# Performance work log

Hardware: AMD Instinct MI355X
Metric: run time of the kernel (lower is better)

## Reference

```python
import jax, jax.numpy as jnp
import numpy as np

N = 100000
DEG = 16            # edges per source node (1 self-loop + 15 random)
E = N * DEG
IN_F = 128
OUT_F = 64
ALPHA = 0.2         # leaky relu negative slope


def _build_edges(key):
    # edges sorted by src (as adj.nonzero() would be), every node has >=1 out-edge
    src = jnp.repeat(jnp.arange(N, dtype=jnp.int32), DEG)
    dst = jax.random.randint(key, (E,), 0, N, dtype=jnp.int32)
    # force a self-loop as the first edge of every block
    self_pos = jnp.arange(E, dtype=jnp.int32) % DEG == 0
    dst = jnp.where(self_pos, src, dst)
    return jnp.stack([src, dst])  # [2, E]


def setup_inputs() -> dict:
    key = jax.random.key(0)
    k1, k2, k3, k4, k5, k6 = jax.random.split(key, 6)
    return {
        "input": jax.random.normal(k1, (N, IN_F), dtype=jnp.float32),
        "edge": _build_edges(k2),
        "W_high": jax.random.normal(k3, (IN_F, OUT_F), dtype=jnp.float32) * 0.1,
        "W_low": jax.random.normal(k4, (IN_F, OUT_F), dtype=jnp.float32) * 0.1,
        "a_high": jax.random.normal(k5, (1, 2 * OUT_F), dtype=jnp.float32) * 0.1,
        "a_low": jax.random.normal(k6, (1, 2 * OUT_F), dtype=jnp.float32) * 0.1,
    }


def _relu6(x):
    return jnp.clip(x, 0.0, 6.0)


def reference(input, edge, W_high, W_low, a_high, a_low):
    n = input.shape[0]
    src, dst = edge[0], edge[1]

    h_high = input @ W_high          # [N, F]
    h_low = input @ W_low            # [N, F]

    # a.mm(cat(h[src], h[dst]).T) == (h @ a_src)[src] + (h @ a_dst)[dst]
    f = W_high.shape[1]
    s_high = (h_high @ a_high[0, :f])[src] + (h_high @ a_high[0, f:])[dst]  # [E]
    s_low = (h_low @ a_low[0, :f])[src] + (h_low @ a_low[0, f:])[dst]

    edge_e_high = jnp.exp(-jax.nn.leaky_relu(s_high, ALPHA))  # [E], > 0
    edge_e_low = jnp.exp(-jax.nn.leaky_relu(s_low, ALPHA))

    seg = lambda v: jax.ops.segment_sum(v, src, num_segments=n, indices_are_sorted=True)

    # rowsum uses RAW exp values (before relu6/dropout), matching the source
    e_high_rowsum = seg(edge_e_high)[:, None]  # [N, 1]
    e_low_rowsum = seg(edge_e_low)[:, None]

    # relu6 clamp (dropout p=0 -> identity, eval mode)
    eh = _relu6(edge_e_high)
    el = _relu6(edge_e_low)

    # m @ (h[src] +/- h[dst]) == segment_sum over src of per-edge features
    h_agg_high = seg(h_high[src] + h_high[dst])   # [N, F]
    h_agg_low = seg(h_low[src] - h_low[dst])      # [N, F]

    # spmm: out[i] = sum_{(i,j)} e_ij * h_agg[j]
    h_prime_high = seg(eh[:, None] * h_agg_high[dst]) / e_high_rowsum
    h_prime_low = seg(el[:, None] * h_agg_low[dst]) / e_low_rowsum

    h_prime = 0.5 * (h_prime_high + h_prime_low)
    return _relu6(h_prime)  # concat=True
```

## Files before the change

kernel.cpp:

```cpp
#include <hip/hip_runtime.h>

#define N_NODES 100000
#define DEG 16
#define IN_F 128
#define OUT_F 64
#define E_EDGES (N_NODES * DEG)

typedef __bf16 bf16x8 __attribute__((ext_vector_type(8)));
typedef unsigned short u16x8 __attribute__((ext_vector_type(8)));
typedef float f32x4 __attribute__((ext_vector_type(4)));

union BF8 { u16x8 u; bf16x8 b; };

__device__ inline float bf2f(unsigned short u) {
    union { unsigned int i; float f; } v; v.i = ((unsigned int)u) << 16; return v.f;
}
__device__ inline unsigned short f2bf(float f) {
    union { float f; unsigned int i; } v; v.f = f;
    unsigned int r = (v.i + 0x7FFFu + ((v.i >> 16) & 1u)) >> 16;
    return (unsigned short)r;
}

__global__ __launch_bounds__(256) void k_gemm(
    const float* __restrict__ in, const float* __restrict__ Wh,
    const float* __restrict__ Wl, unsigned short* __restrict__ h_high,
    unsigned short* __restrict__ h_low)
{
    __shared__ unsigned short ldsW[2][64][136];
    for (int idx = threadIdx.x; idx < IN_F * OUT_F; idx += 256) {
        int k = idx >> 6, n = idx & 63;
        ldsW[0][n][k] = f2bf(Wh[idx]);
        ldsW[1][n][k] = f2bf(Wl[idx]);
    }
    __syncthreads();

    int wave = blockIdx.x * 4 + (threadIdx.x >> 6);
    int lane = threadIdx.x & 63;
    int row0 = wave * 16;
    if (row0 >= N_NODES) return;

    int quad = lane >> 4;
    int mrow = row0 + (lane & 15);
    int lrow = mrow < N_NODES ? mrow : (N_NODES - 1);

    bf16x8 afrag[4];
    const float* inrow = in + (size_t)lrow * IN_F + quad * 8;
    #pragma unroll
    for (int kb = 0; kb < 4; kb++) {
        f32x4 v0 = *(const f32x4*)(inrow + kb * 32);
        f32x4 v1 = *(const f32x4*)(inrow + kb * 32 + 4);
        bf16x8 a;
        #pragma unroll
        for (int j = 0; j < 4; j++) { a[j] = (__bf16)v0[j]; a[4 + j] = (__bf16)v1[j]; }
        afrag[kb] = a;
    }

    f32x4 acc[2][4];
    #pragma unroll
    for (int m = 0; m < 2; m++)
        #pragma unroll
        for (int ct = 0; ct < 4; ct++) acc[m][ct] = (f32x4){0, 0, 0, 0};

    #pragma unroll
    for (int kb = 0; kb < 4; kb++) {
        #pragma unroll
        for (int ct = 0; ct < 4; ct++) {
            int n = ct * 16 + (lane & 15);
            BF8 bh, bl;
            bh.u = *(const u16x8*)&ldsW[0][n][kb * 32 + quad * 8];
            bl.u = *(const u16x8*)&ldsW[1][n][kb * 32 + quad * 8];
            acc[0][ct] = __builtin_amdgcn_mfma_f32_16x16x32_bf16(afrag[kb], bh.b, acc[0][ct], 0, 0, 0);
            acc[1][ct] = __builtin_amdgcn_mfma_f32_16x16x32_bf16(afrag[kb], bl.b, acc[1][ct], 0, 0, 0);
        }
    }

    #pragma unroll
    for (int r = 0; r < 4; r++) {
        int row = row0 + quad * 4 + r;
        if (row >= N_NODES) continue;
        size_t base = (size_t)row * OUT_F + (lane & 15);
        #pragma unroll
        for (int ct = 0; ct < 4; ct++) {
            h_high[base + ct * 16] = f2bf(acc[0][ct][r]);
            h_low [base + ct * 16] = f2bf(acc[1][ct][r]);
        }
    }
}

__global__ __launch_bounds__(256) void k_agg(
    const unsigned short* __restrict__ h_high, const unsigned short* __restrict__ h_low,
    const int* __restrict__ dst, const float* __restrict__ ah, const float* __restrict__ al,
    unsigned short* __restrict__ hagg_h, unsigned short* __restrict__ hagg_l,
    f32x4* __restrict__ s)
{
    int node = blockIdx.x * 4 + (threadIdx.x >> 6);
    if (node >= N_NODES) return;
    int lane = threadIdx.x & 63;

    int jl = dst[node * DEG + (lane & 15)];
    float hh = bf2f(h_high[(size_t)node * 64 + lane]);
    float hl = bf2f(h_low [(size_t)node * 64 + lane]);

    float sh = 16.0f * hh;
    float sl = 16.0f * hl;
    #pragma unroll
    for (int e = 0; e < DEG; e++) {
        int j = __shfl(jl, e);
        sh += bf2f(h_high[(size_t)j * 64 + lane]);
        sl -= bf2f(h_low [(size_t)j * 64 + lane]);
    }
    hagg_h[(size_t)node * 64 + lane] = f2bf(sh);
    hagg_l[(size_t)node * 64 + lane] = f2bf(sl);

    float ph = hh * ah[lane];
    float qh = hh * ah[64 + lane];
    float pl = hl * al[lane];
    float ql = hl * al[64 + lane];
    #pragma unroll
    for (int o = 32; o > 0; o >>= 1) {
        ph += __shfl_xor(ph, o);
        qh += __shfl_xor(qh, o);
        pl += __shfl_xor(pl, o);
        ql += __shfl_xor(ql, o);
    }
    if (lane == 0) s[node] = (f32x4){ph, qh, pl, ql};
}

__global__ __launch_bounds__(256) void k_out(
    const unsigned short* __restrict__ hagg_h, const unsigned short* __restrict__ hagg_l,
    const int* __restrict__ dst, const f32x4* __restrict__ s,
    float* __restrict__ out)
{
    int node = blockIdx.x * 4 + (threadIdx.x >> 6);
    if (node >= N_NODES) return;
    int lane = threadIdx.x & 63;

    int jl = dst[node * DEG + (lane & 15)];
    f32x4 si = s[node];
    float acc_h = 0.0f, acc_l = 0.0f, rs_h = 0.0f, rs_l = 0.0f;
    #pragma unroll
    for (int e = 0; e < DEG; e++) {
        int j = __shfl(jl, e);
        f32x4 sj = s[j];
        float xh = si.x + sj.y;
        float xl = si.z + sj.w;
        float lh = xh > 0.0f ? xh : 0.2f * xh;
        float ll = xl > 0.0f ? xl : 0.2f * xl;
        float wh = __expf(-lh);
        float wl = __expf(-ll);
        rs_h += wh;
        rs_l += wl;
        float eh = fminf(wh, 6.0f);
        float el = fminf(wl, 6.0f);
        acc_h += eh * bf2f(hagg_h[(size_t)j * 64 + lane]);
        acc_l += el * bf2f(hagg_l[(size_t)j * 64 + lane]);
    }
    float r = 0.5f * (acc_h / rs_h + acc_l / rs_l);
    r = fminf(fmaxf(r, 0.0f), 6.0f);
    out[(size_t)node * 64 + lane] = r;
}

extern "C" void kernel_launch(void* const* d_in, const int* in_sizes, int n_in,
                              void* d_out, int out_size, void* d_ws, size_t ws_size,
                              hipStream_t stream) {
    const float* input = (const float*)d_in[0];
    const int*   edge  = (const int*)d_in[1];
    const float* Wh    = (const float*)d_in[2];
    const float* Wl    = (const float*)d_in[3];
    const float* ah    = (const float*)d_in[4];
    const float* al    = (const float*)d_in[5];
    float* out = (float*)d_out;

    unsigned short* h_high = (unsigned short*)d_ws;
    unsigned short* h_low  = h_high + (size_t)N_NODES * 64;
    unsigned short* hagg_h = h_low  + (size_t)N_NODES * 64;
    unsigned short* hagg_l = hagg_h + (size_t)N_NODES * 64;
    f32x4* s = (f32x4*)(hagg_l + (size_t)N_NODES * 64);

    const int* dstp = edge + E_EDGES;

    k_gemm<<<1563, 256, 0, stream>>>(input, Wh, Wl, h_high, h_low);
    k_agg<<<N_NODES / 4, 256, 0, stream>>>(h_high, h_low, dstp, ah, al, hagg_h, hagg_l, s);
    k_out<<<N_NODES / 4, 256, 0, stream>>>(hagg_h, hagg_l, dstp, s, out);
}
```

Measured before the change: 253.1 us.

## Interleave high/low bf16 features into packed words and compute edge weights lane-parallel

Stores h_high and h_low (and the aggregated features) interleaved as packed bf16 pairs in one 32-bit word. Each gathered neighbor row then needs one 256-byte load instead of two separate 128-byte loads, which halves the number of random gather transactions. In k_out, the 16 edge weights and the row sums are now computed once across lanes, with one lane per edge plus a shuffle reduction, instead of being recomputed by every lane inside the loop. The bounds-check early returns are removed, which relies on N being divisible by 4.

```diff
diff --git a/kernel.cpp b/kernel.cpp
--- a/kernel.cpp
+++ b/kernel.cpp
@@ -12,19 +12,23 @@
 
 union BF8 { u16x8 u; bf16x8 b; };
 
-__device__ inline float bf2f(unsigned short u) {
-    union { unsigned int i; float f; } v; v.i = ((unsigned int)u) << 16; return v.f;
+__device__ inline float lo_bf(unsigned int u) {
+    union { unsigned int i; float f; } v; v.i = u << 16; return v.f;
+}
+__device__ inline float hi_bf(unsigned int u) {
+    union { unsigned int i; float f; } v; v.i = u & 0xFFFF0000u; return v.f;
 }
 __device__ inline unsigned short f2bf(float f) {
     union { float f; unsigned int i; } v; v.f = f;
-    unsigned int r = (v.i + 0x7FFFu + ((v.i >> 16) & 1u)) >> 16;
-    return (unsigned short)r;
+    return (unsigned short)((v.i + 0x7FFFu + ((v.i >> 16) & 1u)) >> 16);
+}
+__device__ inline unsigned int packbf(float a, float b) {
+    return (unsigned int)f2bf(a) | ((unsigned int)f2bf(b) << 16);
 }
 
 __global__ __launch_bounds__(256) void k_gemm(
     const float* __restrict__ in, const float* __restrict__ Wh,
-    const float* __restrict__ Wl, unsigned short* __restrict__ h_high,
-    unsigned short* __restrict__ h_low)
+    const float* __restrict__ Wl, unsigned int* __restrict__ H)
 {
     __shared__ unsigned short ldsW[2][64][136];
     for (int idx = threadIdx.x; idx < IN_F * OUT_F; idx += 256) {
@@ -39,8 +43,8 @@
     int row0 = wave * 16;
     if (row0 >= N_NODES) return;
 
-    int quad = lane >> 4;
-    int mrow = row0 + (lane & 15);
+    int quad = lane >> 4, c = lane & 15;
+    int mrow = row0 + c;
     int lrow = mrow < N_NODES ? mrow : (N_NODES - 1);
 
     bf16x8 afrag[4];
@@ -59,18 +63,18 @@
     #pragma unroll
     for (int m = 0; m < 2; m++)
         #pragma unroll
-        for (int ct = 0; ct < 4; ct++) acc[m][ct] = (f32x4){0, 0, 0, 0};
+        for (int t = 0; t < 4; t++) acc[m][t] = (f32x4){0, 0, 0, 0};
 
     #pragma unroll
     for (int kb = 0; kb < 4; kb++) {
         #pragma unroll
-        for (int ct = 0; ct < 4; ct++) {
-            int n = ct * 16 + (lane & 15);
+        for (int t = 0; t < 4; t++) {
+            int n = t * 16 + c;
             BF8 bh, bl;
             bh.u = *(const u16x8*)&ldsW[0][n][kb * 32 + quad * 8];
             bl.u = *(const u16x8*)&ldsW[1][n][kb * 32 + quad * 8];
-            acc[0][ct] = __builtin_amdgcn_mfma_f32_16x16x32_bf16(afrag[kb], bh.b, acc[0][ct], 0, 0, 0);
-            acc[1][ct] = __builtin_amdgcn_mfma_f32_16x16x32_bf16(afrag[kb], bl.b, acc[1][ct], 0, 0, 0);
+            acc[0][t] = __builtin_amdgcn_mfma_f32_16x16x32_bf16(afrag[kb], bh.b, acc[0][t], 0, 0, 0);
+            acc[1][t] = __builtin_amdgcn_mfma_f32_16x16x32_bf16(afrag[kb], bl.b, acc[1][t], 0, 0, 0);
         }
     }
 
@@ -78,39 +82,36 @@
     for (int r = 0; r < 4; r++) {
         int row = row0 + quad * 4 + r;
         if (row >= N_NODES) continue;
-        size_t base = (size_t)row * OUT_F + (lane & 15);
+        size_t base = (size_t)row * OUT_F + c;
         #pragma unroll
-        for (int ct = 0; ct < 4; ct++) {
-            h_high[base + ct * 16] = f2bf(acc[0][ct][r]);
-            h_low [base + ct * 16] = f2bf(acc[1][ct][r]);
-        }
+        for (int t = 0; t < 4; t++)
+            H[base + t * 16] = packbf(acc[0][t][r], acc[1][t][r]);
     }
 }
 
 __global__ __launch_bounds__(256) void k_agg(
-    const unsigned short* __restrict__ h_high, const unsigned short* __restrict__ h_low,
-    const int* __restrict__ dst, const float* __restrict__ ah, const float* __restrict__ al,
-    unsigned short* __restrict__ hagg_h, unsigned short* __restrict__ hagg_l,
-    f32x4* __restrict__ s)
+    const unsigned int* __restrict__ H, const int* __restrict__ dst,
+    const float* __restrict__ ah, const float* __restrict__ al,
+    unsigned int* __restrict__ HAGG, f32x4* __restrict__ s)
 {
     int node = blockIdx.x * 4 + (threadIdx.x >> 6);
-    if (node >= N_NODES) return;
     int lane = threadIdx.x & 63;
 
     int jl = dst[node * DEG + (lane & 15)];
-    float hh = bf2f(h_high[(size_t)node * 64 + lane]);
-    float hl = bf2f(h_low [(size_t)node * 64 + lane]);
+    unsigned int hu = H[(size_t)node * 64 + lane];
+    float hh = lo_bf(hu);
+    float hl = hi_bf(hu);
 
     float sh = 16.0f * hh;
     float sl = 16.0f * hl;
     #pragma unroll
-    for (int e = 0; e < DEG; e++) {
-        int j = __shfl(jl, e);
-        sh += bf2f(h_high[(size_t)j * 64 + lane]);
-        sl -= bf2f(h_low [(size_t)j * 64 + lane]);
+    for (int t = 0; t < DEG; t++) {
+        int j = __shfl(jl, t);
+        unsigned int u = H[(size_t)j * 64 + lane];
+        sh += lo_bf(u);
+        sl -= hi_bf(u);
     }
-    hagg_h[(size_t)node * 64 + lane] = f2bf(sh);
-    hagg_l[(size_t)node * 64 + lane] = f2bf(sl);
+    HAGG[(size_t)node * 64 + lane] = packbf(sh, sl);
 
     float ph = hh * ah[lane];
     float qh = hh * ah[64 + lane];
@@ -127,35 +128,36 @@
 }
 
 __global__ __launch_bounds__(256) void k_out(
-    const unsigned short* __restrict__ hagg_h, const unsigned short* __restrict__ hagg_l,
-    const int* __restrict__ dst, const f32x4* __restrict__ s,
-    float* __restrict__ out)
+    const unsigned int* __restrict__ HAGG, const int* __restrict__ dst,
+    const f32x4* __restrict__ s, float* __restrict__ out)
 {
     int node = blockIdx.x * 4 + (threadIdx.x >> 6);
-    if (node >= N_NODES) return;
     int lane = threadIdx.x & 63;
 
     int jl = dst[node * DEG + (lane & 15)];
     f32x4 si = s[node];
-    float acc_h = 0.0f, acc_l = 0.0f, rs_h = 0.0f, rs_l = 0.0f;
+    f32x4 sj = s[jl];
+    float xh = si.x + sj.y;
+    float xl = si.z + sj.w;
+    float lh = xh > 0.0f ? xh : 0.2f * xh;
+    float ll = xl > 0.0f ? xl : 0.2f * xl;
+    float wh = __expf(-lh);
+    float wl = __expf(-ll);
+    float rh = wh, rl = wl;
     #pragma unroll
-    for (int e = 0; e < DEG; e++) {
-        int j = __shfl(jl, e);
-        f32x4 sj = s[j];
-        float xh = si.x + sj.y;
-        float xl = si.z + sj.w;
-        float lh = xh > 0.0f ? xh : 0.2f * xh;
-        float ll = xl > 0.0f ? xl : 0.2f * xl;
-        float wh = __expf(-lh);
-        float wl = __expf(-ll);
-        rs_h += wh;
-        rs_l += wl;
-        float eh = fminf(wh, 6.0f);
-        float el = fminf(wl, 6.0f);
-        acc_h += eh * bf2f(hagg_h[(size_t)j * 64 + lane]);
-        acc_l += el * bf2f(hagg_l[(size_t)j * 64 + lane]);
+    for (int o = 8; o > 0; o >>= 1) { rh += __shfl_xor(rh, o); rl += __shfl_xor(rl, o); }
+    float eh = fminf(wh, 6.0f);
+    float el = fminf(wl, 6.0f);
+
+    float acc_h = 0.0f, acc_l = 0.0f;
+    #pragma unroll
+    for (int t = 0; t < DEG; t++) {
+        int j = __shfl(jl, t);
+        unsigned int u = HAGG[(size_t)j * 64 + lane];
+        acc_h += __shfl(eh, t) * lo_bf(u);
+        acc_l += __shfl(el, t) * hi_bf(u);
     }
-    float r = 0.5f * (acc_h / rs_h + acc_l / rs_l);
+    float r = 0.5f * (acc_h / rh + acc_l / rl);
     r = fminf(fmaxf(r, 0.0f), 6.0f);
     out[(size_t)node * 64 + lane] = r;
 }
@@ -171,15 +173,13 @@
     const float* al    = (const float*)d_in[5];
     float* out = (float*)d_out;
 
-    unsigned short* h_high = (unsigned short*)d_ws;
-    unsigned short* h_low  = h_high + (size_t)N_NODES * 64;
-    unsigned short* hagg_h = h_low  + (size_t)N_NODES * 64;
-    unsigned short* hagg_l = hagg_h + (size_t)N_NODES * 64;
-    f32x4* s = (f32x4*)(hagg_l + (size_t)N_NODES * 64);
+    unsigned int* H    = (unsigned int*)d_ws;
+    unsigned int* HAGG = H + (size_t)N_NODES * 64;
+    f32x4* s = (f32x4*)(HAGG + (size_t)N_NODES * 64);
 
     const int* dstp = edge + E_EDGES;
 
-    k_gemm<<<1563, 256, 0, stream>>>(input, Wh, Wl, h_high, h_low);
-    k_agg<<<N_NODES / 4, 256, 0, stream>>>(h_high, h_low, dstp, ah, al, hagg_h, hagg_l, s);
-    k_out<<<N_NODES / 4, 256, 0, stream>>>(hagg_h, hagg_l, dstp, s, out);
+    k_gemm<<<1563, 256, 0, stream>>>(input, Wh, Wl, H);
+    k_agg<<<N_NODES / 4, 256, 0, stream>>>(H, dstp, ah, al, HAGG, s);
+    k_out<<<N_NODES / 4, 256, 0, stream>>>(HAGG, dstp, s, out);
 }
```

Result: faster. 233.5 us (-7.7%).
